# Kernel optimization log

Measured on AMD Instinct MI355X. Metric: run time of the kernel, lower is better.

Reference implementation:

```python
import jax, jax.numpy as jnp
import numpy as np

TEMPERATURE = 0.05
EPS = 1e-12  # F.normalize eps


def _l2norm(x):
    n = jnp.sqrt(jnp.sum(x * x, axis=-1, keepdims=True))
    return x / jnp.maximum(n, EPS)


def setup_inputs() -> dict:
    key = jax.random.key(0)
    k1, k2, k3 = jax.random.split(key, 3)
    B, S, D = 8, 1536, 1024
    h1 = jax.random.normal(k1, (B, S, D), dtype=jnp.float32)
    h2 = jax.random.normal(k2, (B, S, D), dtype=jnp.float32)
    mask = jax.random.randint(k3, (B, S), 0, 2).astype(bool)
    return {"last_hidden_states_1": h1, "last_hidden_states_2": h2, "token_mask_batch": mask}


def reference(last_hidden_states_1, last_hidden_states_2, token_mask_batch):
    # Vectorized equivalent of the per-sample python loop: padded (masked) tokens
    # simply contribute nothing to pos/neg sums or the mean.
    B, S, D = last_hidden_states_1.shape
    f1 = _l2norm(last_hidden_states_1)  # [B,S,D]
    f2 = _l2norm(last_hidden_states_2)
    feats = jnp.concatenate([f1, f2], axis=1)  # [B,2S,D]

    # positive pairs: token i in view1 vs token i in view2
    pos_sim = jnp.sum(f1 * f2, axis=-1).astype(jnp.float32) / TEMPERATURE  # [B,S]
    pos = jnp.exp(jnp.concatenate([pos_sim, pos_sim], axis=1))  # [B,2S]

    # all-pairs similarities among the 2n effective tokens
    sim = jnp.einsum("bid,bjd->bij", feats, feats).astype(jnp.float32) / TEMPERATURE  # [B,2S,2S]

    m2 = jnp.concatenate([token_mask_batch, token_mask_batch], axis=1)  # [B,2S]
    tok = jnp.arange(2 * S) % S
    same_token = tok[:, None] == tok[None, :]  # excludes self and its positive counterpart
    neg_mask = m2[:, :, None] & m2[:, None, :] & (~same_token)  # [B,2S,2S]

    Ng = jnp.sum(jnp.exp(sim) * neg_mask, axis=-1)  # [B,2S]
    per_tok = -jnp.log(pos / (Ng + pos))  # [B,2S]

    m2f = m2.astype(jnp.float32)
    per_sample = jnp.sum(per_tok * m2f, axis=1) / jnp.sum(m2f, axis=1)  # mean over 2n tokens
    return jnp.mean(per_sample)
```

## Files before the change

### kernel.cpp

```cpp
#include <hip/hip_runtime.h>
#include <hip/hip_bf16.h>
#include <math.h>

#define BATCH 8
#define SEQ   1536
#define DIM   1024
#define SEQ2  (2*SEQ)
#define TEMP_INV 20.0f
#define EXP_SCALE (TEMP_INV / 64.0f)

#define BM 128
#define BN 128
#define BK 128
#define KITERS (DIM/BK)
#define TILES  (SEQ2 / BM)
#define NPAIRS (TILES * (TILES+1) / 2)

typedef int   i32x4 __attribute__((ext_vector_type(4)));
typedef int   i32x8 __attribute__((ext_vector_type(8)));
typedef float f32x4 __attribute__((ext_vector_type(4)));

#define GLOBAL_AS __attribute__((address_space(1)))
#define LDS_AS    __attribute__((address_space(3)))

__device__ inline void async_ld16(const void* g, void* lds_uniform) {
    __builtin_amdgcn_global_load_lds((const GLOBAL_AS void*)g, (LDS_AS void*)lds_uniform, 16, 0, 0);
}

__device__ inline float wave_red64(float v) {
    #pragma unroll
    for (int m = 32; m > 0; m >>= 1) v += __shfl_xor(v, m, 64);
    return v;
}

__global__ __launch_bounds__(256) void normalize_kernel(
        const float* __restrict__ h1, const float* __restrict__ h2,
        unsigned char* __restrict__ feats, float* __restrict__ pos_cos,
        float* __restrict__ Ng, float* __restrict__ out) {
    int w = threadIdx.x >> 6, lane = threadIdx.x & 63;
    int tok = blockIdx.x * 4 + w;
    int b = tok / SEQ, s = tok - b * SEQ;

    const float4* a4 = (const float4*)(h1 + (size_t)tok * DIM);
    const float4* b4 = (const float4*)(h2 + (size_t)tok * DIM);
    float4 av[4], bv[4];
    #pragma unroll
    for (int it = 0; it < 4; it++) { av[it] = a4[lane + 64*it]; bv[it] = b4[lane + 64*it]; }

    float ss1 = 0.f, ss2 = 0.f, sd = 0.f;
    #pragma unroll
    for (int it = 0; it < 4; it++) {
        ss1 += av[it].x*av[it].x + av[it].y*av[it].y + av[it].z*av[it].z + av[it].w*av[it].w;
        ss2 += bv[it].x*bv[it].x + bv[it].y*bv[it].y + bv[it].z*bv[it].z + bv[it].w*bv[it].w;
        sd  += av[it].x*bv[it].x + av[it].y*bv[it].y + av[it].z*bv[it].z + av[it].w*bv[it].w;
    }
    ss1 = wave_red64(ss1); ss2 = wave_red64(ss2); sd = wave_red64(sd);

    float sc1 = 1.0f / fmaxf(sqrtf(ss1), 1e-12f);
    float sc2 = 1.0f / fmaxf(sqrtf(ss2), 1e-12f);
    float s18 = sc1 * 8.0f, s28 = sc2 * 8.0f;

    unsigned int* f1row = (unsigned int*)(feats + ((size_t)b * SEQ2 + s) * DIM);
    unsigned int* f2row = (unsigned int*)(feats + ((size_t)b * SEQ2 + SEQ + s) * DIM);
    #pragma unroll
    for (int it = 0; it < 4; it++) {
        int p1 = __builtin_amdgcn_cvt_pk_fp8_f32(av[it].x * s18, av[it].y * s18, 0, 0);
        p1     = __builtin_amdgcn_cvt_pk_fp8_f32(av[it].z * s18, av[it].w * s18, p1, 1);
        int p2 = __builtin_amdgcn_cvt_pk_fp8_f32(bv[it].x * s28, bv[it].y * s28, 0, 0);
        p2     = __builtin_amdgcn_cvt_pk_fp8_f32(bv[it].z * s28, bv[it].w * s28, p2, 1);
        f1row[lane + 64*it] = (unsigned int)p1;
        f2row[lane + 64*it] = (unsigned int)p2;
    }
    if (lane == 0) {
        pos_cos[tok] = sd * sc1 * sc2;
        Ng[2*tok] = 0.0f;
        Ng[2*tok + 1] = 0.0f;
        if (tok == 0) out[0] = 0.0f;
    }
}

__global__ __launch_bounds__(256, 3) void gemm_ng_kernel(
        const unsigned char* __restrict__ feats, const int* __restrict__ mask,
        float* __restrict__ Ng) {
    int bid = blockIdx.x;
    int b = bid & 7;
    int p = bid >> 3;
    int ti = 0;
    while (p >= TILES - ti) { p -= TILES - ti; ti++; }
    int tj = ti + p;
    int ibase = ti * BM, jbase = tj * BN;
    bool isdiag = (ti == tj);

    const unsigned char* fb = feats + (size_t)b * SEQ2 * DIM;

    __shared__ __align__(16) unsigned char As[BM][BK];
    __shared__ __align__(16) unsigned char Bs[BN][BK];
    __shared__ float mrow_s[BM];
    __shared__ float mcol_s[BN];

    int t = threadIdx.x;
    int lane = t & 63, w = t >> 6;
    int wrow = w >> 1, wcol = w & 1;
    int colq = lane & 15, quad = lane >> 4;

    int sr = t >> 3;
    int sc = (t & 7) ^ (sr & 7);
    const unsigned char* a0 = fb + (size_t)(ibase + sr) * DIM + sc * 16;
    const unsigned char* b0 = fb + (size_t)(jbase + sr) * DIM + sc * 16;

    auto stage = [&](int it) {
        size_t kb = (size_t)it * BK;
        #pragma unroll
        for (int q = 0; q < 4; q++) {
            async_ld16(a0 + (size_t)q * 32 * DIM + kb, (char*)&As[0][0] + q * 4096 + w * 1024);
            async_ld16(b0 + (size_t)q * 32 * DIM + kb, (char*)&Bs[0][0] + q * 4096 + w * 1024);
        }
    };

    stage(0);

    if (t < BM) {
        int i = ibase + t; int im = (i < SEQ) ? i : i - SEQ;
        mrow_s[t] = mask[b * SEQ + im] ? 1.0f : 0.0f;
    } else {
        int j = jbase + (t - BM); int jm = (j < SEQ) ? j : j - SEQ;
        mcol_s[t - BM] = mask[b * SEQ + jm] ? 1.0f : 0.0f;
    }
    __syncthreads();

    f32x4 acc[4][4] = {};
    int s0 = ((2 * quad)     ^ (colq & 7)) * 16;
    int s1 = ((2 * quad + 1) ^ (colq & 7)) * 16;

    #pragma unroll 1
    for (int it = 0; it < KITERS; it++) {
        i32x8 af[4], bg[4];
        #pragma unroll
        for (int mi = 0; mi < 4; mi++) {
            int row = wrow * 64 + mi * 16 + colq;
            i32x4 lo = *(const i32x4*)&As[row][s0];
            i32x4 hi = *(const i32x4*)&As[row][s1];
            af[mi] = __builtin_shufflevector(lo, hi, 0, 1, 2, 3, 4, 5, 6, 7);
        }
        #pragma unroll
        for (int nj = 0; nj < 4; nj++) {
            int row = wcol * 64 + nj * 16 + colq;
            i32x4 lo = *(const i32x4*)&Bs[row][s0];
            i32x4 hi = *(const i32x4*)&Bs[row][s1];
            bg[nj] = __builtin_shufflevector(lo, hi, 0, 1, 2, 3, 4, 5, 6, 7);
        }

        __syncthreads();

        if (it + 1 < KITERS) {
            stage(it + 1);
            __builtin_amdgcn_sched_barrier(0);
        }

        #pragma unroll
        for (int mi = 0; mi < 4; mi++)
            #pragma unroll
            for (int nj = 0; nj < 4; nj++)
                acc[mi][nj] = __builtin_amdgcn_mfma_scale_f32_16x16x128_f8f6f4(
                    af[mi], bg[nj], acc[mi][nj],
                    0, 0,
                    0, 0x7F7F7F7F,
                    0, 0x7F7F7F7F);

        if (it + 1 < KITERS)
            __syncthreads();
    }

    float mj[4]; int jglob[4];
    #pragma unroll
    for (int nj = 0; nj < 4; nj++) {
        int jl = wcol * 64 + nj * 16 + colq;
        mj[nj] = mcol_s[jl];
        jglob[nj] = jbase + jl;
    }
    float colsum[4] = {0.f, 0.f, 0.f, 0.f};

    #pragma unroll
    for (int mi = 0; mi < 4; mi++) {
        int il0 = wrow * 64 + mi * 16 + quad * 4;
        float rsum[4] = {0.f, 0.f, 0.f, 0.f};
        float mr[4];
        #pragma unroll
        for (int r = 0; r < 4; r++) mr[r] = mrow_s[il0 + r];
        #pragma unroll
        for (int nj = 0; nj < 4; nj++) {
            #pragma unroll
            for (int r = 0; r < 4; r++) {
                int d = (ibase + il0 + r) - jglob[nj];
                bool same = (d == 0) | (d == SEQ) | (d == -SEQ);
                float e = same ? 0.0f : __expf(acc[mi][nj][r] * EXP_SCALE);
                rsum[r] += e * mj[nj];
                colsum[nj] += e * mr[r];
            }
        }
        #pragma unroll
        for (int r = 0; r < 4; r++) {
            float v = rsum[r];
            #pragma unroll
            for (int m = 1; m < 16; m <<= 1) v += __shfl_xor(v, m, 64);
            if (colq == 0)
                atomicAdd(&Ng[b * SEQ2 + ibase + il0 + r], v);
        }
    }

    if (!isdiag) {
        #pragma unroll
        for (int nj = 0; nj < 4; nj++) {
            float v = colsum[nj];
            v += __shfl_xor(v, 16, 64);
            v += __shfl_xor(v, 32, 64);
            if (quad == 0)
                atomicAdd(&Ng[b * SEQ2 + jglob[nj]], v);
        }
    }
}

__global__ __launch_bounds__(1024) void loss_kernel(
        const float* __restrict__ Ng, const float* __restrict__ pos_cos,
        const int* __restrict__ mask, float* __restrict__ out) {
    int b = blockIdx.x, t = threadIdx.x;
    float sum = 0.f, cnt = 0.f;
    for (int i = t; i < SEQ2; i += 1024) {
        int im = (i < SEQ) ? i : i - SEQ;
        if (mask[b * SEQ + im]) {
            float ps = pos_cos[b * SEQ + im] * TEMP_INV;
            float ng = Ng[b * SEQ2 + i];
            sum += log1pf(ng * __expf(-ps));
            cnt += 1.0f;
        }
    }
    sum = wave_red64(sum); cnt = wave_red64(cnt);
    __shared__ float rs[16], rc[16];
    int lane = t & 63, w = t >> 6;
    if (lane == 0) { rs[w] = sum; rc[w] = cnt; }
    __syncthreads();
    if (t == 0) {
        float s = 0.f, c = 0.f;
        #pragma unroll
        for (int k = 0; k < 16; k++) { s += rs[k]; c += rc[k]; }
        atomicAdd(out, s / c * (1.0f / BATCH));
    }
}

extern "C" void kernel_launch(void* const* d_in, const int* in_sizes, int n_in,
                              void* d_out, int out_size, void* d_ws, size_t ws_size,
                              hipStream_t stream) {
    const float* h1  = (const float*)d_in[0];
    const float* h2  = (const float*)d_in[1];
    const int* mask  = (const int*)d_in[2];
    float* out       = (float*)d_out;

    char* ws = (char*)d_ws;
    size_t feats_bytes = (size_t)BATCH * SEQ2 * DIM;
    unsigned char* feats = (unsigned char*)ws;
    float* pos_cos    = (float*)(ws + feats_bytes);
    float* Ng         = (float*)(ws + feats_bytes + (size_t)BATCH * SEQ * 4);

    normalize_kernel<<<BATCH * SEQ / 4, 256, 0, stream>>>(h1, h2, feats, pos_cos, Ng, out);

    gemm_ng_kernel<<<NPAIRS * BATCH, 256, 0, stream>>>(feats, mask, Ng);

    loss_kernel<<<BATCH, 1024, 0, stream>>>(Ng, pos_cos, mask, out);
}
```

Measured before the change: 193.6 us.

## Switch GEMM to 32x32x64 FP8 MFMA with triple-buffered LDS pipeline

Replaces the 16x16x128 scaled MFMA tiling with 32x32x64 instructions, each wave computing a 2x2 grid of 32x32 accumulators. The K loop now uses 64-wide sub-steps with a three-slot LDS ring buffer, prefetching two steps ahead and gating on vmcnt waits with a single barrier per step, instead of double syncthreads. The epilogue is rewritten for the 32x32 accumulator layout, which needs more shuffle reductions and per-row atomics. The aim is better MFMA efficiency and overlap of global loads with compute. The cost is a more complex LDS layout and waitcnt logic that depends on how many loads are in flight.

Result: slower. 219.2 us (+13.2%).

```diff
diff --git a/kernel.cpp b/kernel.cpp
--- a/kernel.cpp
+++ b/kernel.cpp
@@ -11,14 +11,14 @@
 
 #define BM 128
 #define BN 128
-#define BK 128
-#define KITERS (DIM/BK)
+#define SUBK 64
+#define NSUB (DIM/SUBK)
 #define TILES  (SEQ2 / BM)
 #define NPAIRS (TILES * (TILES+1) / 2)
 
 typedef int   i32x4 __attribute__((ext_vector_type(4)));
 typedef int   i32x8 __attribute__((ext_vector_type(8)));
-typedef float f32x4 __attribute__((ext_vector_type(4)));
+typedef float f32x16 __attribute__((ext_vector_type(16)));
 
 #define GLOBAL_AS __attribute__((address_space(1)))
 #define LDS_AS    __attribute__((address_space(3)))
@@ -91,33 +91,33 @@
     int ibase = ti * BM, jbase = tj * BN;
     bool isdiag = (ti == tj);
 
-    const unsigned char* fb = feats + (size_t)b * SEQ2 * DIM;
-
-    __shared__ __align__(16) unsigned char As[BM][BK];
-    __shared__ __align__(16) unsigned char Bs[BN][BK];
+    const unsigned char* fbase = feats + (size_t)b * SEQ2 * DIM;
+
+    __shared__ __align__(16) unsigned char bufs[3][2][64][128];
     __shared__ float mrow_s[BM];
     __shared__ float mcol_s[BN];
 
     int t = threadIdx.x;
     int lane = t & 63, w = t >> 6;
     int wrow = w >> 1, wcol = w & 1;
-    int colq = lane & 15, quad = lane >> 4;
-
-    int sr = t >> 3;
-    int sc = (t & 7) ^ (sr & 7);
-    const unsigned char* a0 = fb + (size_t)(ibase + sr) * DIM + sc * 16;
-    const unsigned char* b0 = fb + (size_t)(jbase + sr) * DIM + sc * 16;
-
-    auto stage = [&](int it) {
-        size_t kb = (size_t)it * BK;
-        #pragma unroll
-        for (int q = 0; q < 4; q++) {
-            async_ld16(a0 + (size_t)q * 32 * DIM + kb, (char*)&As[0][0] + q * 4096 + w * 1024);
-            async_ld16(b0 + (size_t)q * 32 * DIM + kb, (char*)&Bs[0][0] + q * 4096 + w * 1024);
-        }
+
+    int sc_ = (lane & 7) ^ ((lane >> 3) & 7);
+    int sh  = sc_ >> 2, skc = sc_ & 3;
+    const unsigned char* aS = fbase + (size_t)(ibase + 2*(w*8 + (lane>>3)) + sh) * DIM + skc*16;
+    const unsigned char* bS = fbase + (size_t)(jbase + 2*(w*8 + (lane>>3)) + sh) * DIM + skc*16;
+
+    auto stage = [&](int kt, int bi) {
+        size_t kb = (size_t)kt * SUBK;
+        char* la = (char*)&bufs[bi][0][0][0] + w * 1024;
+        char* lb = (char*)&bufs[bi][1][0][0] + w * 1024;
+        async_ld16(aS + kb,                   la);
+        async_ld16(aS + kb + (size_t)64*DIM,  la + 4096);
+        async_ld16(bS + kb,                   lb);
+        async_ld16(bS + kb + (size_t)64*DIM,  lb + 4096);
     };
 
-    stage(0);
+    stage(0, 0);
+    stage(1, 1);
 
     if (t < BM) {
         int i = ibase + t; int im = (i < SEQ) ? i : i - SEQ;
@@ -126,96 +126,87 @@
         int j = jbase + (t - BM); int jm = (j < SEQ) ? j : j - SEQ;
         mcol_s[t - BM] = mask[b * SEQ + jm] ? 1.0f : 0.0f;
     }
-    __syncthreads();
-
-    f32x4 acc[4][4] = {};
-    int s0 = ((2 * quad)     ^ (colq & 7)) * 16;
-    int s1 = ((2 * quad + 1) ^ (colq & 7)) * 16;
+    asm volatile("s_waitcnt vmcnt(4) lgkmcnt(0)" ::: "memory");
+    __builtin_amdgcn_s_barrier();
+    __builtin_amdgcn_sched_barrier(0);
+
+    int hp  = (lane & 31) >> 1;
+    int fc0 = (lane & 1) * 4 + (lane >> 5) * 2;
+    auto rd32 = [&](const unsigned char* part, int pb) -> i32x8 {
+        int pr = pb + hp;
+        int off = pr * 128 + ((fc0 ^ (pr & 7)) << 4);
+        i32x4 lo = *(const i32x4*)(part + off);
+        i32x4 hi = *(const i32x4*)(part + (off ^ 16));
+        return __builtin_shufflevector(lo, hi, 0, 1, 2, 3, 4, 5, 6, 7);
+    };
+
+    f32x16 acc00 = {}, acc01 = {}, acc10 = {}, acc11 = {};
+#define SCL 0x7F7F7F7F
+#define MFMA32(A,B,C) __builtin_amdgcn_mfma_scale_f32_32x32x64_f8f6f4( \
+        A, B, C, 0, 0, 0, SCL, 0, SCL)
 
     #pragma unroll 1
-    for (int it = 0; it < KITERS; it++) {
-        i32x8 af[4], bg[4];
-        #pragma unroll
-        for (int mi = 0; mi < 4; mi++) {
-            int row = wrow * 64 + mi * 16 + colq;
-            i32x4 lo = *(const i32x4*)&As[row][s0];
-            i32x4 hi = *(const i32x4*)&As[row][s1];
-            af[mi] = __builtin_shufflevector(lo, hi, 0, 1, 2, 3, 4, 5, 6, 7);
-        }
-        #pragma unroll
-        for (int nj = 0; nj < 4; nj++) {
-            int row = wcol * 64 + nj * 16 + colq;
-            i32x4 lo = *(const i32x4*)&Bs[row][s0];
-            i32x4 hi = *(const i32x4*)&Bs[row][s1];
-            bg[nj] = __builtin_shufflevector(lo, hi, 0, 1, 2, 3, 4, 5, 6, 7);
-        }
-
-        __syncthreads();
-
-        if (it + 1 < KITERS) {
-            stage(it + 1);
+    for (int k = 0; k < NSUB; k++) {
+        int cur = k % 3;
+        const unsigned char* Ab = &bufs[cur][0][0][0];
+        const unsigned char* Bb = &bufs[cur][1][0][0];
+        i32x8 fA0 = rd32(Ab, wrow * 32);
+        i32x8 fA1 = rd32(Ab, wrow * 32 + 16);
+        i32x8 fB0 = rd32(Bb, wcol * 32);
+        i32x8 fB1 = rd32(Bb, wcol * 32 + 16);
+
+        if (k < NSUB - 2) stage(k + 2, (k + 2) % 3);
+
+        acc00 = MFMA32(fA0, fB0, acc00);
+        acc01 = MFMA32(fA0, fB1, acc01);
+        acc10 = MFMA32(fA1, fB0, acc10);
+        acc11 = MFMA32(fA1, fB1, acc11);
+
+        if (k < NSUB - 2) {
+            asm volatile("s_waitcnt vmcnt(4)" ::: "memory");
+            __builtin_amdgcn_s_barrier();
+            __builtin_amdgcn_sched_barrier(0);
+        } else if (k == NSUB - 2) {
+            asm volatile("s_waitcnt vmcnt(0)" ::: "memory");
+            __builtin_amdgcn_s_barrier();
             __builtin_amdgcn_sched_barrier(0);
         }
-
-        #pragma unroll
-        for (int mi = 0; mi < 4; mi++)
-            #pragma unroll
-            for (int nj = 0; nj < 4; nj++)
-                acc[mi][nj] = __builtin_amdgcn_mfma_scale_f32_16x16x128_f8f6f4(
-                    af[mi], bg[nj], acc[mi][nj],
-                    0, 0,
-                    0, 0x7F7F7F7F,
-                    0, 0x7F7F7F7F);
-
-        if (it + 1 < KITERS)
-            __syncthreads();
-    }
-
-    float mj[4]; int jglob[4];
-    #pragma unroll
-    for (int nj = 0; nj < 4; nj++) {
-        int jl = wcol * 64 + nj * 16 + colq;
-        mj[nj] = mcol_s[jl];
-        jglob[nj] = jbase + jl;
-    }
-    float colsum[4] = {0.f, 0.f, 0.f, 0.f};
-
-    #pragma unroll
-    for (int mi = 0; mi < 4; mi++) {
-        int il0 = wrow * 64 + mi * 16 + quad * 4;
-        float rsum[4] = {0.f, 0.f, 0.f, 0.f};
-        float mr[4];
-        #pragma unroll
-        for (int r = 0; r < 4; r++) mr[r] = mrow_s[il0 + r];
-        #pragma unroll
-        for (int nj = 0; nj < 4; nj++) {
-            #pragma unroll
-            for (int r = 0; r < 4; r++) {
-                int d = (ibase + il0 + r) - jglob[nj];
-                bool same = (d == 0) | (d == SEQ) | (d == -SEQ);
-                float e = same ? 0.0f : __expf(acc[mi][nj][r] * EXP_SCALE);
-                rsum[r] += e * mj[nj];
-                colsum[nj] += e * mr[r];
-            }
-        }
-        #pragma unroll
-        for (int r = 0; r < 4; r++) {
-            float v = rsum[r];
-            #pragma unroll
-            for (int m = 1; m < 16; m <<= 1) v += __shfl_xor(v, m, 64);
-            if (colq == 0)
-                atomicAdd(&Ng[b * SEQ2 + ibase + il0 + r], v);
-        }
-    }
+    }
+
+    int hi = lane >> 5;
+    int bofs = b * SEQ2;
+    float mj0 = mcol_s[wcol * 64 + (lane & 31)];
+    float mj1 = mcol_s[wcol * 64 + 32 + (lane & 31)];
+    int colg0 = jbase + wcol * 64 + (lane & 31);
+    int colg1 = colg0 + 32;
+    float cs0 = 0.f, cs1 = 0.f;
+
+#define EPIROW(A0, A1, MI) do { \
+    _Pragma("unroll") \
+    for (int r = 0; r < 16; r++) { \
+        int rloc = wrow * 64 + (MI) * 32 + (r & 3) + 8 * (r >> 2) + 4 * hi; \
+        int rg = ibase + rloc; \
+        int d0 = rg - colg0, d1 = rg - colg1; \
+        float e0 = ((d0 == 0) | (d0 == SEQ) | (d0 == -SEQ)) ? 0.f : __expf((A0)[r] * EXP_SCALE); \
+        float e1 = ((d1 == 0) | (d1 == SEQ) | (d1 == -SEQ)) ? 0.f : __expf((A1)[r] * EXP_SCALE); \
+        float mr = mrow_s[rloc]; \
+        cs0 += e0 * mr; cs1 += e1 * mr; \
+        float v = e0 * mj0 + e1 * mj1; \
+        v += __shfl_xor(v, 1, 64);  v += __shfl_xor(v, 2, 64); \
+        v += __shfl_xor(v, 4, 64);  v += __shfl_xor(v, 8, 64); \
+        v += __shfl_xor(v, 16, 64); \
+        if ((lane & 31) == 0) atomicAdd(&Ng[bofs + rg], v); \
+    } } while (0)
+
+    EPIROW(acc00, acc01, 0);
+    EPIROW(acc10, acc11, 1);
 
     if (!isdiag) {
-        #pragma unroll
-        for (int nj = 0; nj < 4; nj++) {
-            float v = colsum[nj];
-            v += __shfl_xor(v, 16, 64);
-            v += __shfl_xor(v, 32, 64);
-            if (quad == 0)
-                atomicAdd(&Ng[b * SEQ2 + jglob[nj]], v);
+        cs0 += __shfl_xor(cs0, 32, 64);
+        cs1 += __shfl_xor(cs1, 32, 64);
+        if (hi == 0) {
+            atomicAdd(&Ng[bofs + colg0], cs0);
+            atomicAdd(&Ng[bofs + colg1], cs1);
         }
     }
 }
```

## Load A fragments directly from global and double-buffer B tile in LDS

Applied to the files above, without the earlier changes.

The A operand is now read straight from global memory into registers in MFMA fragment layout, so it no longer needs an LDS staging buffer. The freed LDS holds a double-buffered B tile. With that, the per-iteration sync becomes a single vmcnt wait plus barrier instead of two __syncthreads. The aim is to halve LDS traffic and overlap the next B prefetch with compute. The cost is uncoalesced 16-byte per-lane global loads for A, whose latency is exposed each iteration with no prefetch.

Result: slower. 226.9 us (+17.2%).

```diff
diff --git a/kernel.cpp b/kernel.cpp
--- a/kernel.cpp
+++ b/kernel.cpp
@@ -93,8 +93,7 @@
 
     const unsigned char* fb = feats + (size_t)b * SEQ2 * DIM;
 
-    __shared__ __align__(16) unsigned char As[BM][BK];
-    __shared__ __align__(16) unsigned char Bs[BN][BK];
+    __shared__ __align__(16) unsigned char Bs[2][BN][BK];
     __shared__ float mrow_s[BM];
     __shared__ float mcol_s[BN];
 
@@ -105,19 +104,17 @@
 
     int sr = t >> 3;
     int sc = (t & 7) ^ (sr & 7);
-    const unsigned char* a0 = fb + (size_t)(ibase + sr) * DIM + sc * 16;
     const unsigned char* b0 = fb + (size_t)(jbase + sr) * DIM + sc * 16;
 
-    auto stage = [&](int it) {
+    auto stageB = [&](int it, int d) {
         size_t kb = (size_t)it * BK;
-        #pragma unroll
-        for (int q = 0; q < 4; q++) {
-            async_ld16(a0 + (size_t)q * 32 * DIM + kb, (char*)&As[0][0] + q * 4096 + w * 1024);
-            async_ld16(b0 + (size_t)q * 32 * DIM + kb, (char*)&Bs[0][0] + q * 4096 + w * 1024);
-        }
+        char* base = (char*)&Bs[d][0][0];
+        #pragma unroll
+        for (int q = 0; q < 4; q++)
+            async_ld16(b0 + (size_t)q * 32 * DIM + kb, base + q * 4096 + w * 1024);
     };
 
-    stage(0);
+    stageB(0, 0);
 
     if (t < BM) {
         int i = ibase + t; int im = (i < SEQ) ? i : i - SEQ;
@@ -128,47 +125,57 @@
     }
     __syncthreads();
 
+    const unsigned char* aG0 = fb + (size_t)(ibase + wrow*64      + colq) * DIM + quad * 32;
+    const unsigned char* aG1 = aG0 + (size_t)16 * DIM;
+    const unsigned char* aG2 = aG0 + (size_t)32 * DIM;
+    const unsigned char* aG3 = aG0 + (size_t)48 * DIM;
+
     f32x4 acc[4][4] = {};
     int s0 = ((2 * quad)     ^ (colq & 7)) * 16;
     int s1 = ((2 * quad + 1) ^ (colq & 7)) * 16;
 
     #pragma unroll 1
     for (int it = 0; it < KITERS; it++) {
-        i32x8 af[4], bg[4];
-        #pragma unroll
-        for (int mi = 0; mi < 4; mi++) {
-            int row = wrow * 64 + mi * 16 + colq;
-            i32x4 lo = *(const i32x4*)&As[row][s0];
-            i32x4 hi = *(const i32x4*)&As[row][s1];
-            af[mi] = __builtin_shufflevector(lo, hi, 0, 1, 2, 3, 4, 5, 6, 7);
-        }
+        size_t kb = (size_t)it * BK;
+        i32x4 al0 = *(const i32x4*)(aG0 + kb);
+        i32x4 ah0 = *(const i32x4*)(aG0 + kb + 16);
+        i32x4 al1 = *(const i32x4*)(aG1 + kb);
+        i32x4 ah1 = *(const i32x4*)(aG1 + kb + 16);
+        i32x4 al2 = *(const i32x4*)(aG2 + kb);
+        i32x4 ah2 = *(const i32x4*)(aG2 + kb + 16);
+        i32x4 al3 = *(const i32x4*)(aG3 + kb);
+        i32x4 ah3 = *(const i32x4*)(aG3 + kb + 16);
+        __builtin_amdgcn_sched_barrier(0);
+        if (it + 1 < KITERS) stageB(it + 1, (it + 1) & 1);
+        __builtin_amdgcn_sched_barrier(0);
+        i32x8 bg[4];
         #pragma unroll
         for (int nj = 0; nj < 4; nj++) {
             int row = wcol * 64 + nj * 16 + colq;
-            i32x4 lo = *(const i32x4*)&Bs[row][s0];
-            i32x4 hi = *(const i32x4*)&Bs[row][s1];
+            const unsigned char* rp = &Bs[it & 1][row][0];
+            i32x4 lo = *(const i32x4*)(rp + s0);
+            i32x4 hi = *(const i32x4*)(rp + s1);
             bg[nj] = __builtin_shufflevector(lo, hi, 0, 1, 2, 3, 4, 5, 6, 7);
         }
-
-        __syncthreads();
-
+        i32x8 af0 = __builtin_shufflevector(al0, ah0, 0, 1, 2, 3, 4, 5, 6, 7);
+        i32x8 af1 = __builtin_shufflevector(al1, ah1, 0, 1, 2, 3, 4, 5, 6, 7);
+        i32x8 af2 = __builtin_shufflevector(al2, ah2, 0, 1, 2, 3, 4, 5, 6, 7);
+        i32x8 af3 = __builtin_shufflevector(al3, ah3, 0, 1, 2, 3, 4, 5, 6, 7);
+        #pragma unroll
+        for (int nj = 0; nj < 4; nj++) {
+            acc[0][nj] = __builtin_amdgcn_mfma_scale_f32_16x16x128_f8f6f4(
+                af0, bg[nj], acc[0][nj], 0, 0, 0, 0x7F7F7F7F, 0, 0x7F7F7F7F);
+            acc[1][nj] = __builtin_amdgcn_mfma_scale_f32_16x16x128_f8f6f4(
+                af1, bg[nj], acc[1][nj], 0, 0, 0, 0x7F7F7F7F, 0, 0x7F7F7F7F);
+            acc[2][nj] = __builtin_amdgcn_mfma_scale_f32_16x16x128_f8f6f4(
+                af2, bg[nj], acc[2][nj], 0, 0, 0, 0x7F7F7F7F, 0, 0x7F7F7F7F);
+            acc[3][nj] = __builtin_amdgcn_mfma_scale_f32_16x16x128_f8f6f4(
+                af3, bg[nj], acc[3][nj], 0, 0, 0, 0x7F7F7F7F, 0, 0x7F7F7F7F);
+        }
         if (it + 1 < KITERS) {
-            stage(it + 1);
-            __builtin_amdgcn_sched_barrier(0);
-        }
-
-        #pragma unroll
-        for (int mi = 0; mi < 4; mi++)
-            #pragma unroll
-            for (int nj = 0; nj < 4; nj++)
-                acc[mi][nj] = __builtin_amdgcn_mfma_scale_f32_16x16x128_f8f6f4(
-                    af[mi], bg[nj], acc[mi][nj],
-                    0, 0,
-                    0, 0x7F7F7F7F,
-                    0, 0x7F7F7F7F);
-
-        if (it + 1 < KITERS)
-            __syncthreads();
+            asm volatile("s_waitcnt vmcnt(0)" ::: "memory");
+            __builtin_amdgcn_s_barrier();
+        }
     }
 
     float mj[4]; int jglob[4];
```

## Double-buffer B tile and prefetch two K-steps ahead with explicit waitcnts

Applied to the files above, without the earlier changes.

Splits the async staging of A and B tiles and gives B a second LDS buffer, so B for iteration it+2 is loaded while A for it+1 is loaded. __syncthreads is replaced by explicit s_waitcnt vmcnt/lgkmcnt plus raw s_barrier, letting some global loads stay in flight across barriers. This is meant to hide more global-load latency behind the MFMA loop. It costs 16KB more LDS per block, which may reduce occupancy against the launch bound of 3 blocks. The hand-counted vmcnt values are fragile and must match the real number of outstanding loads.

Result: slower. 199.9 us (+3.3%).

```diff
diff --git a/kernel.cpp b/kernel.cpp
--- a/kernel.cpp
+++ b/kernel.cpp
@@ -94,7 +94,7 @@
     const unsigned char* fb = feats + (size_t)b * SEQ2 * DIM;
 
     __shared__ __align__(16) unsigned char As[BM][BK];
-    __shared__ __align__(16) unsigned char Bs[BN][BK];
+    __shared__ __align__(16) unsigned char Bs[2][BN][BK];
     __shared__ float mrow_s[BM];
     __shared__ float mcol_s[BN];
 
@@ -108,16 +108,22 @@
     const unsigned char* a0 = fb + (size_t)(ibase + sr) * DIM + sc * 16;
     const unsigned char* b0 = fb + (size_t)(jbase + sr) * DIM + sc * 16;
 
-    auto stage = [&](int it) {
+    auto stageA = [&](int it) {
         size_t kb = (size_t)it * BK;
         #pragma unroll
-        for (int q = 0; q < 4; q++) {
+        for (int q = 0; q < 4; q++)
             async_ld16(a0 + (size_t)q * 32 * DIM + kb, (char*)&As[0][0] + q * 4096 + w * 1024);
-            async_ld16(b0 + (size_t)q * 32 * DIM + kb, (char*)&Bs[0][0] + q * 4096 + w * 1024);
-        }
     };
-
-    stage(0);
+    auto stageB = [&](int it, int d) {
+        size_t kb = (size_t)it * BK;
+        #pragma unroll
+        for (int q = 0; q < 4; q++)
+            async_ld16(b0 + (size_t)q * 32 * DIM + kb, (char*)&Bs[d][0][0] + q * 4096 + w * 1024);
+    };
+
+    stageB(0, 0);
+    stageA(0);
+    stageB(1, 1);
 
     if (t < BM) {
         int i = ibase + t; int im = (i < SEQ) ? i : i - SEQ;
@@ -126,7 +132,8 @@
         int j = jbase + (t - BM); int jm = (j < SEQ) ? j : j - SEQ;
         mcol_s[t - BM] = mask[b * SEQ + jm] ? 1.0f : 0.0f;
     }
-    __syncthreads();
+    asm volatile("s_waitcnt vmcnt(4) lgkmcnt(0)" ::: "memory");
+    __builtin_amdgcn_s_barrier();
 
     f32x4 acc[4][4] = {};
     int s0 = ((2 * quad)     ^ (colq & 7)) * 16;
@@ -145,17 +152,18 @@
         #pragma unroll
         for (int nj = 0; nj < 4; nj++) {
             int row = wcol * 64 + nj * 16 + colq;
-            i32x4 lo = *(const i32x4*)&Bs[row][s0];
-            i32x4 hi = *(const i32x4*)&Bs[row][s1];
+            const unsigned char* rp = &Bs[it & 1][row][0];
+            i32x4 lo = *(const i32x4*)(rp + s0);
+            i32x4 hi = *(const i32x4*)(rp + s1);
             bg[nj] = __builtin_shufflevector(lo, hi, 0, 1, 2, 3, 4, 5, 6, 7);
         }
 
-        __syncthreads();
-
-        if (it + 1 < KITERS) {
-            stage(it + 1);
-            __builtin_amdgcn_sched_barrier(0);
-        }
+        asm volatile("s_waitcnt lgkmcnt(0)" ::: "memory");
+        __builtin_amdgcn_s_barrier();
+
+        if (it + 1 < KITERS) stageA(it + 1);
+        if (it + 2 < KITERS) stageB(it + 2, it & 1);
+        __builtin_amdgcn_sched_barrier(0);
 
         #pragma unroll
         for (int mi = 0; mi < 4; mi++)
@@ -167,8 +175,13 @@
                     0, 0x7F7F7F7F,
                     0, 0x7F7F7F7F);
 
-        if (it + 1 < KITERS)
-            __syncthreads();
+        if (it + 1 < KITERS) {
+            if (it + 2 < KITERS)
+                asm volatile("s_waitcnt vmcnt(4)" ::: "memory");
+            else
+                asm volatile("s_waitcnt vmcnt(0)" ::: "memory");
+            __builtin_amdgcn_s_barrier();
+        }
     }
 
     float mj[4]; int jglob[4];
```
